# Kernel tuning notes

Measured on AMD Instinct MI355X. Metric: run time of the kernel, lower is better.

Reference implementation:

```python
import jax, jax.numpy as jnp
import numpy as np

B, S, D, H, DFF = 4, 1024, 1024, 16, 4096
DK = D // H
EPS = 1e-5

def _ln(x, g, b):
    m = jnp.mean(x, -1, keepdims=True)
    v = jnp.mean((x - m) ** 2, -1, keepdims=True)
    return (x - m) * jax.lax.rsqrt(v + EPS) * g + b

def setup_inputs() -> dict:
    key = jax.random.key(0)
    ks = jax.random.split(key, 24)
    std = 0.02
    def w(k, shp):
        return jax.random.normal(k, shp, jnp.float32) * std
    return {
        'x': jax.random.normal(ks[0], (B, S, D), jnp.float32),
        'wq': w(ks[1], (D, D)), 'bq': jnp.zeros((D,), jnp.float32),
        'wk': w(ks[2], (D, D)), 'bk': jnp.zeros((D,), jnp.float32),
        'wv': w(ks[3], (D, D)), 'bv': jnp.zeros((D,), jnp.float32),
        'wo': w(ks[4], (D, D)), 'bo': jnp.zeros((D,), jnp.float32),
        'rel_table': jax.random.normal(ks[5], (2 * 64 - 1, H), jnp.float32),
        'g1': jnp.ones((D,), jnp.float32), 'be1': jnp.zeros((D,), jnp.float32),
        'g2': jnp.ones((D,), jnp.float32), 'be2': jnp.zeros((D,), jnp.float32),
        'w1': w(ks[6], (D, DFF)), 'b1': jnp.zeros((DFF,), jnp.float32),
        'w2': w(ks[7], (DFF, D)), 'b2': jnp.zeros((D,), jnp.float32),
        'w3': w(ks[8], (D, D)), 'b3': jnp.zeros((D,), jnp.float32),
        'gf': jnp.ones((D,), jnp.float32), 'bf': jnp.zeros((D,), jnp.float32),
    }

def reference(x, wq, bq, wk, bk, wv, bv, wo, bo, rel_table,
              g1, be1, g2, be2, w1, b1, w2, b2, w3, b3, gf, bf):
    # --- pre-norm attention ---
    nx = _ln(x, g1, be1)
    def heads(w, b):
        return (nx @ w + b).reshape(B, S, H, DK).transpose(0, 2, 1, 3)  # [B,H,S,DK]
    Q, K, V = heads(wq, bq), heads(wk, bk), heads(wv, bv)
    scores = jnp.einsum('bhsd,bhtd->bhst', Q, K) / jnp.sqrt(jnp.float32(DK))
    # relative position bias, clamped to table range
    rel = jnp.arange(S)[None, :] - jnp.arange(S)[:, None] + 63
    rel = jnp.clip(rel, 0, 2 * 64 - 2)               # [S,S]
    bias = rel_table[rel].transpose(2, 0, 1)          # [H,S,S]
    scores = scores + bias[None]
    attn = jax.nn.softmax(scores, axis=-1)
    ctx = jnp.einsum('bhst,bhtd->bhsd', attn, V)
    ctx = ctx.transpose(0, 2, 1, 3).reshape(B, S, D)
    x = x + (ctx @ wo + bo)
    # --- feed-forward (with its own inner residuals) ---
    nx2 = _ln(x, g2, be2)
    ff1 = jax.nn.gelu(nx2 @ w1 + b1, approximate=False) @ w2 + b2
    y = nx2 + ff1
    ff2 = _ln(y, gf, bf) @ w3 + b3
    ff_out = y + ff2
    return x + ff_out
```

## Files before the change

### kernel.cpp

```cpp
#include <hip/hip_runtime.h>
#include <hip/hip_bf16.h>
#include <math.h>


constexpr int Bc = 4, Sc_ = 1024, Dc = 1024, Hc = 16, DKc = 64, DFFc = 4096;
constexpr int ROWS = Bc * Sc_;
constexpr int BK = 32;

typedef short short8 __attribute__((ext_vector_type(8)));
typedef __bf16 bf16x8 __attribute__((ext_vector_type(8)));
typedef float float4v __attribute__((ext_vector_type(4)));
typedef uint uint2v __attribute__((ext_vector_type(2)));

__device__ __forceinline__ float bf2f(ushort u) {
    union { uint i; float f; } v; v.i = ((uint)u) << 16; return v.f;
}
__device__ __forceinline__ ushort f2bf(float f) {
    union { float f; uint i; } v; v.f = f;
    uint r = v.i + 0x7FFF + ((v.i >> 16) & 1);
    return (ushort)(r >> 16);
}
__device__ __forceinline__ bf16x8 as_bf(short8 s) {
    union { short8 s; bf16x8 b; } u; u.s = s; return u.b;
}
__device__ __forceinline__ uint cvt_pk_bf16(float lo, float hi) {
    uint r;
    asm("v_cvt_pk_bf16_f32 %0, %1, %2" : "=v"(r) : "v"(lo), "v"(hi));
    return r;
}
__device__ __forceinline__ float exp2_hw(float x) {
    float r;
    asm("v_exp_f32 %0, %1" : "=v"(r) : "v"(x));
    return r;
}
__device__ __forceinline__ void async_copy16(void* lds, const void* g) {
    __builtin_amdgcn_global_load_lds((const __attribute__((address_space(1))) uint*)g,
                                     (__attribute__((address_space(3))) uint*)lds, 16, 0, 0);
}
__device__ __forceinline__ float gelu_f(float v) {
    float z = v * 0.70710678118654752f;
    float az = fabsf(z);
    float t = 1.f / (1.f + 0.3275911f * az);
    float p = ((((1.061405429f * t - 1.453152027f) * t) + 1.421413741f) * t
               - 0.284496736f) * t + 0.254829592f;
    float y = 1.f - p * t * __expf(-az * az);
    float er = (z < 0.f) ? -y : y;
    return 0.5f * v * (1.f + er);
}

__global__ void sentinel_kernel(float* __restrict__ out, int n) {
    int i = blockIdx.x * 256 + threadIdx.x;
    if (i < n) out[i] = 100.0f;
}

__global__ void bias3_kernel(const float* __restrict__ a, const float* __restrict__ b,
                             const float* __restrict__ c, float* __restrict__ o) {
    int i = blockIdx.x * 256 + threadIdx.x;
    if (i < 1024) o[i] = a[i];
    else if (i < 2048) o[i] = b[i - 1024];
    else if (i < 3072) o[i] = c[i - 2048];
}

__global__ __launch_bounds__(256) void wconv_kernel(const float* __restrict__ W,
                                                    ushort* __restrict__ Wt,
                                                    int K, int N) {
    __shared__ float T[64][65];
    const int kt = blockIdx.y * 64, nt = blockIdx.x * 64;
    const int tid = threadIdx.x;
#pragma unroll
    for (int it = 0; it < 4; it++) {
        int r = it * 16 + (tid >> 4), c = (tid & 15) * 4;
        float4v v = *reinterpret_cast<const float4v*>(W + (size_t)(kt + r) * N + nt + c);
        T[r][c] = v[0]; T[r][c + 1] = v[1]; T[r][c + 2] = v[2]; T[r][c + 3] = v[3];
    }
    __syncthreads();
    int n = tid >> 2, kc = (tid & 3) * 16;
    short8 a, b;
#pragma unroll
    for (int q = 0; q < 8; q++) {
        a[q] = (short)f2bf(T[kc + q][n]);
        b[q] = (short)f2bf(T[kc + 8 + q][n]);
    }
    ushort* dst = Wt + (size_t)(nt + n) * K + kt + kc;
    *reinterpret_cast<short8*>(dst) = a;
    *reinterpret_cast<short8*>(dst + 8) = b;
}

__global__ __launch_bounds__(256) void vconv_kernel(const ushort* __restrict__ V,
                                                    ushort* __restrict__ Vt) {
    __shared__ ushort T[64][65];
    const int bh = blockIdx.y;
    const int s0 = blockIdx.x * 64;
    const int tid = threadIdx.x;
    const int r = tid >> 2, c = (tid & 3) * 16;
    const ushort* src = V + ((size_t)bh * Sc_ + s0 + r) * DKc + c;
    short8 a = *reinterpret_cast<const short8*>(src);
    short8 b = *reinterpret_cast<const short8*>(src + 8);
#pragma unroll
    for (int q = 0; q < 8; q++) { T[r][c + q] = (ushort)a[q]; T[r][c + 8 + q] = (ushort)b[q]; }
    __syncthreads();
    const int dk = tid >> 2, sc2 = (tid & 3) * 16;
    short8 o0, o1;
#pragma unroll
    for (int q = 0; q < 8; q++) { o0[q] = (short)T[sc2 + q][dk]; o1[q] = (short)T[sc2 + 8 + q][dk]; }
    ushort* dst = Vt + ((size_t)bh * DKc + dk) * Sc_ + s0 + sc2;
    *reinterpret_cast<short8*>(dst) = o0;
    *reinterpret_cast<short8*>(dst + 8) = o1;
}

template<bool IN_F32>
__global__ __launch_bounds__(256) void ln_kernel(const void* __restrict__ xin,
                                                 const float* __restrict__ g,
                                                 const float* __restrict__ be,
                                                 ushort* __restrict__ out) {
    int row = blockIdx.x;
    int tid = threadIdx.x;
    float v0[4], s = 0.f, ss = 0.f;
#pragma unroll
    for (int i = 0; i < 4; i++) {
        int c = tid + i * 256;
        float f = IN_F32 ? ((const float*)xin)[(size_t)row * Dc + c]
                         : bf2f(((const ushort*)xin)[(size_t)row * Dc + c]);
        v0[i] = f; s += f; ss += f * f;
    }
#pragma unroll
    for (int off = 32; off > 0; off >>= 1) {
        s += __shfl_down(s, off);
        ss += __shfl_down(ss, off);
    }
    __shared__ float red[8];
    __shared__ float stat[2];
    int wave = tid >> 6, lane = tid & 63;
    if (lane == 0) { red[wave] = s; red[wave + 4] = ss; }
    __syncthreads();
    if (tid == 0) {
        float a = 0.f, b = 0.f;
        for (int w = 0; w < 4; w++) { a += red[w]; b += red[w + 4]; }
        stat[0] = a; stat[1] = b;
    }
    __syncthreads();
    float mean = stat[0] * (1.f / Dc);
    float var  = stat[1] * (1.f / Dc) - mean * mean;
    float inv  = rsqrtf(var + 1e-5f);
#pragma unroll
    for (int i = 0; i < 4; i++) {
        int c = tid + i * 256;
        float nv = (v0[i] - mean) * inv * g[c] + be[c];
        out[(size_t)row * Dc + c] = f2bf(nv);
    }
}

template<int BM, int BN, typename OutT>
__global__ __launch_bounds__(256) void gemm_bt(
    const ushort* __restrict__ Ag, const ushort* __restrict__ Wt,
    const float* __restrict__ biasg,
    const float* __restrict__ res1f,
    const ushort* __restrict__ resi1, const ushort* __restrict__ resi2,
    OutT* __restrict__ outg,
    int M, int N, int K, int do_gelu, int mode) {
    constexpr int WN = BN / 64;
    constexpr int WM = 4 / WN;
    constexpr int MI = BM / (WM * 16);
    constexpr int TSZ = (BM + BN) * BK;
    constexpr int TOT = (BM + BN) * 4;
    __shared__ ushort Tile[2 * TSZ];
    const int tid = threadIdx.x;
    const int wave = tid >> 6, lane = tid & 63;
    const int quad = lane >> 4, l16 = lane & 15;
    const int m0 = blockIdx.x * BM, n0 = blockIdx.y * BN;
    const int wm = (wave / WN) * (MI * 16), wn = (wave % WN) * 64;

    float4v acc[MI][4];
    const float4v zero = {0.f, 0.f, 0.f, 0.f};
#pragma unroll
    for (int i = 0; i < MI; i++)
#pragma unroll
        for (int j = 0; j < 4; j++) acc[i][j] = zero;

    auto stage = [&](int buf, int k0) {
#pragma unroll
        for (int it = 0; it < TOT / 256; it++) {
            int c = tid + it * 256;
            int row = c >> 2, kc = (c & 3) * 8;
            const ushort* src = (row < BM)
                ? Ag + (size_t)(m0 + row) * K + k0 + kc
                : Wt + (size_t)(n0 + row - BM) * K + k0 + kc;
            async_copy16(&Tile[buf * TSZ + c * 8], src);
        }
    };

    const int nit = K / BK;
    stage(0, 0);
    for (int i = 0; i < nit; i++) {
        int buf = i & 1;
        __builtin_amdgcn_sched_barrier(0);
        __builtin_amdgcn_s_waitcnt(0x0F70);
        __builtin_amdgcn_s_barrier();
        __builtin_amdgcn_sched_barrier(0);
        if (i + 1 < nit) stage(buf ^ 1, (i + 1) * BK);
        __builtin_amdgcn_sched_barrier(0);
        const ushort* Asb = &Tile[buf * TSZ];
        const ushort* Bsb = &Tile[buf * TSZ + BM * BK];
        short8 af[MI], bfr[4];
#pragma unroll
        for (int ii = 0; ii < MI; ii++)
            af[ii] = *reinterpret_cast<const short8*>(&Asb[(wm + ii * 16 + l16) * BK + quad * 8]);
#pragma unroll
        for (int j = 0; j < 4; j++)
            bfr[j] = *reinterpret_cast<const short8*>(&Bsb[(wn + j * 16 + l16) * BK + quad * 8]);
#pragma unroll
        for (int j = 0; j < 4; j++)
#pragma unroll
            for (int ii = 0; ii < MI; ii++)
                acc[ii][j] = __builtin_amdgcn_mfma_f32_16x16x32_bf16(as_bf(af[ii]), as_bf(bfr[j]), acc[ii][j], 0, 0, 0);
    }
    __builtin_amdgcn_s_barrier();

#pragma unroll
    for (int j = 0; j < 4; j++) {
        int cg = n0 + wn + j * 16 + l16;
        float bv = biasg ? biasg[cg] : 0.f;
#pragma unroll
        for (int i = 0; i < MI; i++) {
#pragma unroll
            for (int r = 0; r < 4; r++) {
                int rg = m0 + wm + i * 16 + quad * 4 + r;
                float v = acc[i][j][r] + bv;
                if (do_gelu) v = gelu_f(v);
                size_t idx = (size_t)rg * N + cg;
                if (res1f) v += res1f[idx];
                if (resi1) v += bf2f(resi1[idx]);
                if (resi2) v += bf2f(resi2[idx]);
                size_t dst;
                if (mode == 1) {
                    int which = cg >> 10, wr2 = cg & 1023;
                    int h = wr2 >> 6, dk = wr2 & 63;
                    int b = rg >> 10, s = rg & 1023;
                    dst = (size_t)which * ((size_t)ROWS * Dc)
                        + (((size_t)b * Hc + h) * Sc_ + s) * DKc + dk;
                } else dst = idx;
                if constexpr (sizeof(OutT) == 4) outg[dst] = v;
                else                             outg[dst] = f2bf(v);
            }
        }
    }
}

__global__ __launch_bounds__(256, 4) void attn_kernel(
    const ushort* __restrict__ Qg, const ushort* __restrict__ Kg,
    const ushort* __restrict__ Vt, const float* __restrict__ relg,
    ushort* __restrict__ ctxg) {
    __shared__ ushort Kl[2][2048];
    __shared__ ushort Vl[2][2048];
    __shared__ float Tpad[1088];
    constexpr float L2E = 1.44269504f;

    const int blk = blockIdx.x;
    const int vb = (blk & 7) * 128 + (blk >> 3);
    const int bh = vb >> 4;
    const int qblk = vb & 15;
    const int h = bh & (Hc - 1);
    const int b = bh >> 4;
    const int qb = qblk * 64;
    const int tid = threadIdx.x;
    const int wave = tid >> 6, lane = tid & 63;
    const int quad = lane >> 4, l16 = lane & 15;
    const int ql = wave * 16 + l16;

    const ushort* Kbh  = Kg + (size_t)bh * Sc_ * DKc;
    const ushort* Vtbh = Vt + (size_t)bh * DKc * Sc_;

    auto stage = [&](int buf, int t0) {
        {
            int r = tid >> 3, ch = tid & 7;
            const ushort* src = Kbh + (size_t)(t0 + r) * DKc + ((ch ^ (r & 7)) * 8);
            async_copy16(&Kl[buf][tid * 8], src);
        }
        {
            int d = tid >> 2, ch = tid & 3;
            const ushort* src = Vtbh + (size_t)d * Sc_ + t0 + ((ch ^ ((d >> 1) & 3)) * 8);
            async_copy16(&Vl[buf][tid * 8], src);
        }
    };

    stage(0, 0);

    for (int j = tid; j < 1087; j += 256) {
        int r = min(max(j - qb, 0), 126);
        Tpad[j] = relg[r * Hc + h];
    }

    short8 aQ[2];
    {
        const ushort* qrow = Qg + ((size_t)bh * Sc_ + qb + ql) * DKc + quad * 8;
#pragma unroll
        for (int f = 0; f < 2; f++) {
            short8 v = *reinterpret_cast<const short8*>(qrow + f * 32);
#pragma unroll
            for (int e = 0; e < 8; e++) v[e] = (short)f2bf(bf2f((ushort)v[e]) * 0.125f);
            aQ[f] = v;
        }
    }
    __syncthreads();

    float4v accO[4];
#pragma unroll
    for (int i = 0; i < 4; i++) accO[i] = float4v{0.f, 0.f, 0.f, 0.f};
    float m = -1e30f, lsum = 0.f;
    float ml2 = m * L2E;
    const int srcA = ((quad & 1) * 2) * 16 + l16;
    const int srcB = srcA + 16;
    const bool hi = quad >= 2;

    auto compute = [&](int buf, int t0) {
        short8 vf[4];
#pragma unroll
        for (int dt = 0; dt < 4; dt++) {
            int d = dt * 16 + l16;
            vf[dt] = *reinterpret_cast<const short8*>(
                &Vl[buf][d * 32 + ((quad ^ ((l16 >> 1) & 3)) * 8)]);
        }
        short8 kf[2][2];
#pragma unroll
        for (int kt = 0; kt < 2; kt++)
#pragma unroll
            for (int f = 0; f < 2; f++)
                kf[kt][f] = *reinterpret_cast<const short8*>(
                    &Kl[buf][(kt * 16 + l16) * 64 + (((f * 4 + quad) ^ (l16 & 7)) * 8)]);

        const int jb = t0 + quad * 4 - ql + 63;
        float4v c0 = { Tpad[jb],      Tpad[jb + 1],  Tpad[jb + 2],  Tpad[jb + 3]  };
        float4v c1 = { Tpad[jb + 16], Tpad[jb + 17], Tpad[jb + 18], Tpad[jb + 19] };

        float4v s0 = __builtin_amdgcn_mfma_f32_16x16x32_bf16(as_bf(kf[0][0]), as_bf(aQ[0]), c0, 0, 0, 0);
        s0 = __builtin_amdgcn_mfma_f32_16x16x32_bf16(as_bf(kf[0][1]), as_bf(aQ[1]), s0, 0, 0, 0);
        float4v s1 = __builtin_amdgcn_mfma_f32_16x16x32_bf16(as_bf(kf[1][0]), as_bf(aQ[0]), c1, 0, 0, 0);
        s1 = __builtin_amdgcn_mfma_f32_16x16x32_bf16(as_bf(kf[1][1]), as_bf(aQ[1]), s1, 0, 0, 0);

        float lt = fmaxf(fmaxf(fmaxf(s0[0], s0[1]), fmaxf(s0[2], s0[3])),
                         fmaxf(fmaxf(s1[0], s1[1]), fmaxf(s1[2], s1[3])));
        if (!__all(lt <= m + 8.f)) {
            float tmax = fmaxf(lt, __shfl_xor(lt, 16));
            tmax = fmaxf(tmax, __shfl_xor(tmax, 32));
            float mn = fmaxf(m, tmax);
            float sc = exp2_hw((m - mn) * L2E);
            m = mn; ml2 = m * L2E;
            lsum *= sc;
#pragma unroll
            for (int dt = 0; dt < 4; dt++)
#pragma unroll
                for (int r = 0; r < 4; r++) accO[dt][r] *= sc;
        }
        float p0[4], p1[4];
#pragma unroll
        for (int r = 0; r < 4; r++) {
            p0[r] = exp2_hw(fmaf(s0[r], L2E, -ml2));
            p1[r] = exp2_hw(fmaf(s1[r], L2E, -ml2));
        }
        lsum += ((p0[0] + p0[1]) + (p0[2] + p0[3]))
              + ((p1[0] + p1[1]) + (p1[2] + p1[3]));

        uint w0 = cvt_pk_bf16(p0[0], p0[1]);
        uint w1 = cvt_pk_bf16(p0[2], p0[3]);
        uint w2 = cvt_pk_bf16(p1[0], p1[1]);
        uint w3 = cvt_pk_bf16(p1[2], p1[3]);
        uint a0 = __shfl(w0, srcA), a1 = __shfl(w1, srcA);
        uint a2 = __shfl(w2, srcA), a3 = __shfl(w3, srcA);
        uint b0 = __shfl(w0, srcB), b1 = __shfl(w1, srcB);
        uint b2 = __shfl(w2, srcB), b3 = __shfl(w3, srcB);
        union { uint u[4]; short8 s; } pf;
        pf.u[0] = hi ? a2 : a0;
        pf.u[1] = hi ? a3 : a1;
        pf.u[2] = hi ? b2 : b0;
        pf.u[3] = hi ? b3 : b1;

#pragma unroll
        for (int dt = 0; dt < 4; dt++)
            accO[dt] = __builtin_amdgcn_mfma_f32_16x16x32_bf16(as_bf(vf[dt]), as_bf(pf.s), accO[dt], 0, 0, 0);
    };

    for (int t0 = 0; t0 < Sc_; t0 += 64) {
        __builtin_amdgcn_sched_barrier(0);
        __builtin_amdgcn_s_waitcnt(0x0F70);
        __builtin_amdgcn_s_barrier();
        __builtin_amdgcn_sched_barrier(0);
        stage(1, t0 + 32);
        __builtin_amdgcn_sched_barrier(0);
        compute(0, t0);

        __builtin_amdgcn_sched_barrier(0);
        __builtin_amdgcn_s_waitcnt(0x0F70);
        __builtin_amdgcn_s_barrier();
        __builtin_amdgcn_sched_barrier(0);
        if (t0 + 64 < Sc_) stage(0, t0 + 64);
        __builtin_amdgcn_sched_barrier(0);
        compute(1, t0 + 32);
    }

    lsum += __shfl_xor(lsum, 16);
    lsum += __shfl_xor(lsum, 32);
    float linv = 1.f / lsum;

    const int s = qb + ql;
    ushort* orow = ctxg + ((size_t)b * Sc_ + s) * Dc + h * DKc + quad * 4;
#pragma unroll
    for (int dt = 0; dt < 4; dt++) {
        uint2v o;
        o[0] = cvt_pk_bf16(accO[dt][0] * linv, accO[dt][1] * linv);
        o[1] = cvt_pk_bf16(accO[dt][2] * linv, accO[dt][3] * linv);
        *reinterpret_cast<uint2v*>(orow + dt * 16) = o;
    }
}

extern "C" void kernel_launch(void* const* d_in, const int* in_sizes, int n_in,
                              void* d_out, int out_size, void* d_ws, size_t ws_size,
                              hipStream_t stream) {
    float* out = (float*)d_out;

    static const int exp_sizes[22] = {
        4194304, 1048576, 1024, 1048576, 1024, 1048576, 1024, 1048576, 1024,
        2032, 1024, 1024, 1024, 1024, 4194304, 4096, 4194304, 1024,
        1048576, 1024, 1024, 1024};
    bool ok = (n_in == 22);
    if (ok) for (int i = 0; i < 22; i++) if (in_sizes[i] != exp_sizes[i]) { ok = false; break; }
    if (!ok) {
        sentinel_kernel<<<(out_size + 255) / 256, 256, 0, stream>>>(out, out_size);
        return;
    }

    const float* x   = (const float*)d_in[0];
    const float* wq  = (const float*)d_in[1];  const float* bq  = (const float*)d_in[2];
    const float* wk  = (const float*)d_in[3];  const float* bk  = (const float*)d_in[4];
    const float* wv  = (const float*)d_in[5];  const float* bv  = (const float*)d_in[6];
    const float* wo  = (const float*)d_in[7];  const float* bo  = (const float*)d_in[8];
    const float* rel = (const float*)d_in[9];
    const float* g1  = (const float*)d_in[10]; const float* be1 = (const float*)d_in[11];
    const float* g2  = (const float*)d_in[12]; const float* be2 = (const float*)d_in[13];
    const float* w1  = (const float*)d_in[14]; const float* b1  = (const float*)d_in[15];
    const float* w2  = (const float*)d_in[16]; const float* b2  = (const float*)d_in[17];
    const float* w3  = (const float*)d_in[18]; const float* b3  = (const float*)d_in[19];
    const float* gf  = (const float*)d_in[20]; const float* bfp = (const float*)d_in[21];

    constexpr size_t NE = (size_t)ROWS * Dc;
    ushort* base = (ushort*)d_ws;
    ushort* Wts  = base;
    ushort* nx   = base + NE;
    ushort* Qb   = base + 2 * NE;
    ushort* Kb   = base + 3 * NE;
    ushort* Vb   = base + 4 * NE;
    ushort* Vt   = base + 5 * NE;
    float*  bqkv = (float*)(base + 6 * NE);
    ushort* ctx  = nx;
    ushort* x1   = Qb;
    ushort* nx2  = Kb;
    ushort* hb   = base + 4 * NE;
    ushort* yb   = nx;
    ushort* ly   = Kb;

    dim3 blk(256);
    dim3 gQKV(ROWS / 64, 3072 / 128);
    dim3 gD(ROWS / 64, Dc / 128);
    dim3 gFF(ROWS / 128, DFFc / 128);
    dim3 cD(Dc / 64, Dc / 64);
    dim3 c1(DFFc / 64, Dc / 64);
    dim3 c2(Dc / 64, DFFc / 64);
    dim3 cV(Sc_ / 64, Bc * Hc);

    ln_kernel<true><<<ROWS, blk, 0, stream>>>(x, g1, be1, nx);
    wconv_kernel<<<cD, blk, 0, stream>>>(wq, Wts, Dc, Dc);
    wconv_kernel<<<cD, blk, 0, stream>>>(wk, Wts + (size_t)1024 * 1024, Dc, Dc);
    wconv_kernel<<<cD, blk, 0, stream>>>(wv, Wts + (size_t)2048 * 1024, Dc, Dc);
    bias3_kernel<<<12, blk, 0, stream>>>(bq, bk, bv, bqkv);
    gemm_bt<64, 128, ushort><<<gQKV, blk, 0, stream>>>(nx, Wts, bqkv, nullptr, nullptr, nullptr, Qb, ROWS, 3072, Dc, 0, 1);
    vconv_kernel<<<cV, blk, 0, stream>>>(Vb, Vt);
    attn_kernel<<<dim3(1024), blk, 0, stream>>>(Qb, Kb, Vt, rel, ctx);
    wconv_kernel<<<cD, blk, 0, stream>>>(wo, Wts, Dc, Dc);
    gemm_bt<64, 128, ushort><<<gD, blk, 0, stream>>>(ctx, Wts, bo, x, nullptr, nullptr, x1, ROWS, Dc, Dc, 0, 0);
    ln_kernel<false><<<ROWS, blk, 0, stream>>>(x1, g2, be2, nx2);
    wconv_kernel<<<c1, blk, 0, stream>>>(w1, Wts, Dc, DFFc);
    gemm_bt<128, 128, ushort><<<gFF, blk, 0, stream>>>(nx2, Wts, b1, nullptr, nullptr, nullptr, hb, ROWS, DFFc, Dc, 1, 0);
    wconv_kernel<<<c2, blk, 0, stream>>>(w2, Wts, DFFc, Dc);
    gemm_bt<64, 128, ushort><<<gD, blk, 0, stream>>>(hb, Wts, b2, nullptr, nx2, nullptr, yb, ROWS, Dc, DFFc, 0, 0);
    ln_kernel<false><<<ROWS, blk, 0, stream>>>(yb, gf, bfp, ly);
    wconv_kernel<<<cD, blk, 0, stream>>>(w3, Wts, Dc, Dc);
    gemm_bt<64, 128, float><<<gD, blk, 0, stream>>>(ly, Wts, b3, nullptr, x1, yb, out, ROWS, Dc, Dc, 0, 0);
}
```

Baseline: 442.1 us.

## Add 256x256-tile 8-wave GEMM with quarter-staged async pipeline for QKV and FF1

Introduces a new bf16 MFMA GEMM kernel using 512 threads and 256x256 output tiles, with a BK=64 double-buffered shared-memory pipeline that stages the A and B halves in four quarter steps interleaved with compute. It uses XOR-swizzled LDS layout, explicit waitcnt/barrier scheduling and setprio around the MFMA bursts. The kernel replaces the smaller-tile GEMMs for the QKV projection and the first FFN layer, aiming for more data reuse per loaded tile and better overlap of loads with math. In exchange it uses much more LDS and registers per block and launches fewer blocks, which may hurt occupancy or tail balance.

```diff
diff --git a/kernel.cpp b/kernel.cpp
--- a/kernel.cpp
+++ b/kernel.cpp
@@ -246,6 +246,127 @@
     }
 }
 
+template<typename OutT>
+__global__ __launch_bounds__(512, 2) void gemm8_bt(
+    const ushort* __restrict__ Ag, const ushort* __restrict__ Wt,
+    const float* __restrict__ biasg, OutT* __restrict__ outg,
+    int N, int K, int do_gelu, int mode) {
+    __shared__ ushort Al[2][16384];
+    __shared__ ushort Bl[2][16384];
+    const int tid = threadIdx.x;
+    const int wave = tid >> 6, lane = tid & 63;
+    const int quad = lane >> 4, l16 = lane & 15;
+    const int wm = (wave >> 2) * 128, wn = (wave & 3) * 64;
+    const int m0 = blockIdx.y * 256, n0 = blockIdx.x * 256;
+
+    float4v acc[8][4];
+    const float4v zero = {0.f, 0.f, 0.f, 0.f};
+#pragma unroll
+    for (int i = 0; i < 8; i++)
+#pragma unroll
+        for (int j = 0; j < 4; j++) acc[i][j] = zero;
+
+    auto stageH = [&](int buf, int k0, int which) {
+#pragma unroll
+        for (int it = 0; it < 2; it++) {
+            int s = tid + it * 512;
+            int rl = s >> 3, pch = s & 7;
+            int ch = pch ^ (rl & 7);
+            const ushort* src; ushort* dst;
+            if (which == 0)      { int row = ((rl >> 6) << 7) + (rl & 63);
+                                   src = Ag + (size_t)(m0 + row) * K + k0 + ch * 8;
+                                   dst = &Al[buf][s * 8]; }
+            else if (which == 1) { int row = ((rl >> 5) << 6) + (rl & 31);
+                                   src = Wt + (size_t)(n0 + row) * K + k0 + ch * 8;
+                                   dst = &Bl[buf][s * 8]; }
+            else if (which == 2) { int row = ((rl >> 5) << 6) + 32 + (rl & 31);
+                                   src = Wt + (size_t)(n0 + row) * K + k0 + ch * 8;
+                                   dst = &Bl[buf][8192 + s * 8]; }
+            else                 { int row = ((rl >> 6) << 7) + 64 + (rl & 63);
+                                   src = Ag + (size_t)(m0 + row) * K + k0 + ch * 8;
+                                   dst = &Al[buf][8192 + s * 8]; }
+            async_copy16(dst, src);
+        }
+    };
+
+    const int rlA = ((wm >> 7) << 6) + l16;
+    const int rlB = ((wn >> 6) << 5) + l16;
+    const int sw  = l16 & 7;
+
+    const int nt = K >> 6;
+    stageH(0, 0, 0); stageH(0, 0, 1); stageH(0, 0, 2); stageH(0, 0, 3);
+
+#define G8_SYNC(WHICH, VMLAST)                                            \
+    __builtin_amdgcn_sched_barrier(0);                                    \
+    if (more) { stageH(nbuf, knext, WHICH);                               \
+                __builtin_amdgcn_sched_barrier(0);                        \
+                __builtin_amdgcn_s_waitcnt(0x0F76);         \
+    } else   { __builtin_amdgcn_s_waitcnt(VMLAST); }                      \
+    __builtin_amdgcn_s_barrier();                                         \
+    __builtin_amdgcn_sched_barrier(0);
+
+#define G8_COMPUTE(QM, QN, LOADA)                                         \
+    if (LOADA) {                                                          \
+        _Pragma("unroll") for (int kk = 0; kk < 2; kk++)                  \
+        _Pragma("unroll") for (int i = 0; i < 4; i++)                     \
+            af[kk][i] = *reinterpret_cast<const short8*>(                 \
+                &Al[buf][(QM) * 8192 + (rlA + i * 16) * 64 +              \
+                         (((kk << 2) | quad) ^ sw) * 8]);                 \
+    }                                                                     \
+    _Pragma("unroll") for (int kk = 0; kk < 2; kk++)                      \
+    _Pragma("unroll") for (int j = 0; j < 2; j++)                         \
+        bfr[kk][j] = *reinterpret_cast<const short8*>(                    \
+            &Bl[buf][(QN) * 8192 + (rlB + j * 16) * 64 +                  \
+                     (((kk << 2) | quad) ^ sw) * 8]);                     \
+    __builtin_amdgcn_s_setprio(1);                                        \
+    _Pragma("unroll") for (int kk = 0; kk < 2; kk++)                      \
+    _Pragma("unroll") for (int i = 0; i < 4; i++)                         \
+    _Pragma("unroll") for (int j = 0; j < 2; j++)                         \
+        acc[(QM) * 4 + i][(QN) * 2 + j] =                                 \
+            __builtin_amdgcn_mfma_f32_16x16x32_bf16(                      \
+                as_bf(af[kk][i]), as_bf(bfr[kk][j]),                      \
+                acc[(QM) * 4 + i][(QN) * 2 + j], 0, 0, 0);                \
+    __builtin_amdgcn_s_setprio(0);
+
+    for (int t = 0; t < nt; ++t) {
+        const int buf = t & 1, nbuf = buf ^ 1;
+        const int knext = (t + 1) << 6;
+        const bool more = (t + 1 < nt);
+        short8 af[2][4], bfr[2][2];
+        G8_SYNC(0, 0x0F74)  G8_COMPUTE(0, 0, true)
+        G8_SYNC(1, 0x0F72)  G8_COMPUTE(0, 1, false)
+        G8_SYNC(2, 0x0F70)  G8_COMPUTE(1, 0, true)
+        G8_SYNC(3, 0x0F70)  G8_COMPUTE(1, 1, false)
+    }
+#undef G8_SYNC
+#undef G8_COMPUTE
+
+#pragma unroll
+    for (int jg = 0; jg < 4; jg++) {
+        int cg = n0 + wn + jg * 16 + l16;
+        float bv = biasg ? biasg[cg] : 0.f;
+#pragma unroll
+        for (int ig = 0; ig < 8; ig++) {
+#pragma unroll
+            for (int r = 0; r < 4; r++) {
+                int rg = m0 + wm + ig * 16 + quad * 4 + r;
+                float v = acc[ig][jg][r] + bv;
+                if (do_gelu) v = gelu_f(v);
+                size_t dst;
+                if (mode == 1) {
+                    int which = cg >> 10, wr2 = cg & 1023;
+                    int h = wr2 >> 6, dk = wr2 & 63;
+                    int b = rg >> 10, s = rg & 1023;
+                    dst = (size_t)which * ((size_t)ROWS * Dc)
+                        + (((size_t)b * Hc + h) * Sc_ + s) * DKc + dk;
+                } else dst = (size_t)rg * N + cg;
+                if constexpr (sizeof(OutT) == 4) outg[dst] = v;
+                else                             outg[dst] = f2bf(v);
+            }
+        }
+    }
+}
+
 __global__ __launch_bounds__(256, 4) void attn_kernel(
     const ushort* __restrict__ Qg, const ushort* __restrict__ Kg,
     const ushort* __restrict__ Vt, const float* __restrict__ relg,
@@ -458,9 +579,10 @@
     ushort* ly   = Kb;
 
     dim3 blk(256);
-    dim3 gQKV(ROWS / 64, 3072 / 128);
+    dim3 blk8(512);
+    dim3 gQKV(3072 / 256, ROWS / 256);
     dim3 gD(ROWS / 64, Dc / 128);
-    dim3 gFF(ROWS / 128, DFFc / 128);
+    dim3 gFF(DFFc / 256, ROWS / 256);
     dim3 cD(Dc / 64, Dc / 64);
     dim3 c1(DFFc / 64, Dc / 64);
     dim3 c2(Dc / 64, DFFc / 64);
@@ -471,14 +593,14 @@
     wconv_kernel<<<cD, blk, 0, stream>>>(wk, Wts + (size_t)1024 * 1024, Dc, Dc);
     wconv_kernel<<<cD, blk, 0, stream>>>(wv, Wts + (size_t)2048 * 1024, Dc, Dc);
     bias3_kernel<<<12, blk, 0, stream>>>(bq, bk, bv, bqkv);
-    gemm_bt<64, 128, ushort><<<gQKV, blk, 0, stream>>>(nx, Wts, bqkv, nullptr, nullptr, nullptr, Qb, ROWS, 3072, Dc, 0, 1);
+    gemm8_bt<ushort><<<gQKV, blk8, 0, stream>>>(nx, Wts, bqkv, Qb, 3072, Dc, 0, 1);
     vconv_kernel<<<cV, blk, 0, stream>>>(Vb, Vt);
     attn_kernel<<<dim3(1024), blk, 0, stream>>>(Qb, Kb, Vt, rel, ctx);
     wconv_kernel<<<cD, blk, 0, stream>>>(wo, Wts, Dc, Dc);
     gemm_bt<64, 128, ushort><<<gD, blk, 0, stream>>>(ctx, Wts, bo, x, nullptr, nullptr, x1, ROWS, Dc, Dc, 0, 0);
     ln_kernel<false><<<ROWS, blk, 0, stream>>>(x1, g2, be2, nx2);
     wconv_kernel<<<c1, blk, 0, stream>>>(w1, Wts, Dc, DFFc);
-    gemm_bt<128, 128, ushort><<<gFF, blk, 0, stream>>>(nx2, Wts, b1, nullptr, nullptr, nullptr, hb, ROWS, DFFc, Dc, 1, 0);
+    gemm8_bt<ushort><<<gFF, blk8, 0, stream>>>(nx2, Wts, b1, hb, DFFc, Dc, 1, 0);
     wconv_kernel<<<c2, blk, 0, stream>>>(w2, Wts, DFFc, Dc);
     gemm_bt<64, 128, ushort><<<gD, blk, 0, stream>>>(hb, Wts, b2, nullptr, nx2, nullptr, yb, ROWS, Dc, DFFc, 0, 0);
     ln_kernel<false><<<ROWS, blk, 0, stream>>>(yb, gf, bfp, ly);
```

New measurement: 451.4 us. +2.1%, slower.
